# Performance work log

Measured on AMD Instinct MI355X. Metric: run time of the kernel, lower is better.

Reference implementation:

```python
import jax, jax.numpy as jnp
import numpy as np

EMBED = 768
HEADS = 12
HEAD_DIM = EMBED // HEADS
HIDDEN = int(EMBED * 4.0)
EPS = 1e-5


def setup_inputs() -> dict:
    key = jax.random.key(0)
    ks = jax.random.split(key, 12)
    s = 0.02
    return {
        "x": jax.random.normal(ks[0], (8, 1024, EMBED), dtype=jnp.float32),
        # norm1 / norm2 (LayerNorm affine params)
        "g1": jnp.ones((EMBED,), jnp.float32),
        "b1": jnp.zeros((EMBED,), jnp.float32),
        "g2": jnp.ones((EMBED,), jnp.float32),
        "b2": jnp.zeros((EMBED,), jnp.float32),
        # attention weights (stored [in, out]; qkv_bias=False)
        "w_qkv": jax.random.normal(ks[1], (EMBED, 3 * EMBED), jnp.float32) * s,
        "w_proj": jax.random.normal(ks[2], (EMBED, EMBED), jnp.float32) * s,
        "b_proj": jnp.zeros((EMBED,), jnp.float32),
        # MLP weights
        "w_fc1": jax.random.normal(ks[3], (EMBED, HIDDEN), jnp.float32) * s,
        "b_fc1": jnp.zeros((HIDDEN,), jnp.float32),
        "w_fc2": jax.random.normal(ks[4], (HIDDEN, EMBED), jnp.float32) * s,
        "b_fc2": jnp.zeros((EMBED,), jnp.float32),
    }


def _layernorm(x, g, b):
    mu = jnp.mean(x, axis=-1, keepdims=True)
    var = jnp.var(x, axis=-1, keepdims=True)
    return (x - mu) * jax.lax.rsqrt(var + EPS) * g + b


def reference(x, g1, b1, g2, b2, w_qkv, w_proj, b_proj, w_fc1, b_fc1, w_fc2, b_fc2):
    B, N, C = x.shape
    scaling = HEAD_DIM ** (-0.5)

    # --- attention branch ---
    h = _layernorm(x, g1, b1)
    qkv = (h @ w_qkv).reshape(B, N, 3, HEADS, HEAD_DIM)
    q, k, v = qkv[:, :, 0], qkv[:, :, 1], qkv[:, :, 2]  # [B, N, H, D]
    attn = jnp.einsum("bnhd,bmhd->bhnm", q, k) * scaling  # full NxN scores
    attn = jax.nn.softmax(attn, axis=-1)
    out = jnp.einsum("bhnm,bmhd->bnhd", attn, v).reshape(B, N, C)
    out = out @ w_proj + b_proj
    x = x + out

    # --- MLP branch ---
    h = _layernorm(x, g2, b2)
    h = jax.nn.gelu(h @ w_fc1 + b_fc1, approximate=False)
    h = h @ w_fc2 + b_fc2
    return x + h
```

## Files before the change

### kernel.cpp

```cpp
#include <hip/hip_runtime.h>
#include <hip/hip_bf16.h>
#include <math.h>

#define EMBED 768
#define HEADS 12
#define HEAD_DIM 64
#define HIDDEN 3072
#define SEQ 1024
#define BATCH 8
#define TOKENS (SEQ*BATCH)

typedef unsigned short u16;
typedef __attribute__((ext_vector_type(8))) short bf16x8;
typedef __attribute__((ext_vector_type(4))) float floatx4;
typedef __attribute__((ext_vector_type(4))) u16 u16x4;
typedef __attribute__((ext_vector_type(2))) u16 u16x2;

__device__ __forceinline__ u16 f2bf(float f){
    union { float f; unsigned u; } v; v.f = f;
    unsigned r = v.u + 0x7fffu + ((v.u >> 16) & 1u);
    return (u16)(r >> 16);
}

__device__ __forceinline__ unsigned cvt_pk_bf16(float lo, float hi){
    unsigned r;
    asm("v_cvt_pk_bf16_f32 %0, %1, %2" : "=v"(r) : "v"(lo), "v"(hi));
    return r;
}

__device__ __forceinline__ void gload16(const void* g, void* l){
    __builtin_amdgcn_global_load_lds((const __attribute__((address_space(1))) void*)g,
                                     (__attribute__((address_space(3))) void*)l, 16, 0, 0);
}

__device__ __forceinline__ float gelu_fast(float x){
    float t = 1.5957691216f * (x + 0.044715f * x * x * x);
    return x / (1.0f + __expf(-t));
}

__global__ __launch_bounds__(256) void prep_kernel(const float* __restrict__ w0, const float* __restrict__ w1,
                                   const float* __restrict__ w2, const float* __restrict__ w3,
                                   u16* __restrict__ o0, u16* __restrict__ o1,
                                   u16* __restrict__ o2, u16* __restrict__ o3,
                                   const float* __restrict__ x, const float* __restrict__ g,
                                   const float* __restrict__ bln, u16* __restrict__ lnout){
    int bb = blockIdx.x;
    int tid = threadIdx.x;
    if(bb >= 6912){
        int row  = (bb - 6912) * 4 + (tid >> 6);
        int lane = tid & 63;
        const float4* xr = (const float4*)(x + (size_t)row * EMBED);
        float4 v[3];
        float s = 0.f;
        #pragma unroll
        for(int i=0;i<3;i++){
            v[i] = xr[i*64 + lane];
            s += v[i].x + v[i].y + v[i].z + v[i].w;
        }
        #pragma unroll
        for(int o=32;o>0;o>>=1) s += __shfl_xor(s, o);
        float mu = s * (1.0f/EMBED);
        float s2 = 0.f;
        #pragma unroll
        for(int i=0;i<3;i++){
            float dx = v[i].x-mu, dy = v[i].y-mu, dz = v[i].z-mu, dw = v[i].w-mu;
            s2 += dx*dx + dy*dy + dz*dz + dw*dw;
        }
        #pragma unroll
        for(int o=32;o>0;o>>=1) s2 += __shfl_xor(s2, o);
        float rstd = rsqrtf(s2*(1.0f/EMBED) + 1e-5f);
        u16* orow = lnout + (size_t)row * EMBED;
        const float4* g4 = (const float4*)g;
        const float4* b4 = (const float4*)bln;
        #pragma unroll
        for(int i=0;i<3;i++){
            int c4 = i*64 + lane;
            float4 gv = g4[c4], bv = b4[c4];
            u16x4 pk;
            pk.x = f2bf((v[i].x-mu)*rstd*gv.x + bv.x);
            pk.y = f2bf((v[i].y-mu)*rstd*gv.y + bv.y);
            pk.z = f2bf((v[i].z-mu)*rstd*gv.z + bv.z);
            pk.w = f2bf((v[i].w-mu)*rstd*gv.w + bv.w);
            *(u16x4*)(orow + c4*4) = pk;
        }
        return;
    }
    const float* W; u16* Wt; int K, N, bx, by;
    if(bb < 1728)      { int l = bb;        W=w0; Wt=o0; K=768;  N=2304; bx=l%72; by=l/72; }
    else if(bb < 2304) { int l = bb-1728;   W=w1; Wt=o1; K=768;  N=768;  bx=l%24; by=l/24; }
    else if(bb < 4608) { int l = bb-2304;   W=w2; Wt=o2; K=768;  N=3072; bx=l%96; by=l/96; }
    else               { int l = bb-4608;   W=w3; Wt=o3; K=3072; N=768;  bx=l%24; by=l/24; }

    __shared__ float tile[32][33];
    int n0 = bx * 32, k0 = by * 32;
    int tx = tid & 31, ty = tid >> 5;
    #pragma unroll
    for(int i=0;i<32;i+=8) tile[ty+i][tx] = W[(size_t)(k0+ty+i)*N + n0+tx];
    __syncthreads();
    int kp = (tid & 15)*2, nn = tid >> 4;
    #pragma unroll
    for(int p=0;p<2;p++){
        int n = nn + p*16;
        u16x2 w2v;
        w2v.x = f2bf(tile[kp  ][n]);
        w2v.y = f2bf(tile[kp+1][n]);
        *(u16x2*)(Wt + (size_t)(n0+n)*K + k0 + kp) = w2v;
    }
}

__global__ __launch_bounds__(256) void ln_kernel(const float* __restrict__ x, const float* __restrict__ g,
                                                 const float* __restrict__ b, u16* __restrict__ out){
    int row  = blockIdx.x * 4 + (threadIdx.x >> 6);
    int lane = threadIdx.x & 63;
    const float4* xr = (const float4*)(x + (size_t)row * EMBED);
    float4 v[3];
    float s = 0.f;
    #pragma unroll
    for(int i=0;i<3;i++){
        v[i] = xr[i*64 + lane];
        s += v[i].x + v[i].y + v[i].z + v[i].w;
    }
    #pragma unroll
    for(int o=32;o>0;o>>=1) s += __shfl_xor(s, o);
    float mu = s * (1.0f/EMBED);
    float s2 = 0.f;
    #pragma unroll
    for(int i=0;i<3;i++){
        float dx = v[i].x-mu, dy = v[i].y-mu, dz = v[i].z-mu, dw = v[i].w-mu;
        s2 += dx*dx + dy*dy + dz*dz + dw*dw;
    }
    #pragma unroll
    for(int o=32;o>0;o>>=1) s2 += __shfl_xor(s2, o);
    float rstd = rsqrtf(s2*(1.0f/EMBED) + 1e-5f);
    u16* orow = out + (size_t)row * EMBED;
    const float4* g4 = (const float4*)g;
    const float4* b4 = (const float4*)b;
    #pragma unroll
    for(int i=0;i<3;i++){
        int c4 = i*64 + lane;
        float4 gv = g4[c4], bv = b4[c4];
        u16x4 pk;
        pk.x = f2bf((v[i].x-mu)*rstd*gv.x + bv.x);
        pk.y = f2bf((v[i].y-mu)*rstd*gv.y + bv.y);
        pk.z = f2bf((v[i].z-mu)*rstd*gv.z + bv.z);
        pk.w = f2bf((v[i].w-mu)*rstd*gv.w + bv.w);
        *(u16x4*)(orow + c4*4) = pk;
    }
}

template<int EPI>
__global__ __launch_bounds__(512,4) void gemm_wide(const u16* __restrict__ A, const u16* __restrict__ Bt,
        void* __restrict__ Cout, const float* __restrict__ bias, const float* __restrict__ res,
        u16* __restrict__ vt, int M, int N, int K, int ldc){
    __shared__ __align__(16) u16 As[128*64];
    __shared__ __align__(16) u16 Bs[2*256*64];
    int tid  = threadIdx.x;
    int wave = tid >> 6, lane = tid & 63;
    int quad = lane >> 4, lm = lane & 15;
    int wm = (wave >> 2) * 64;
    int wn = (wave & 3) * 64;

    int gx = gridDim.x;
    int bid = blockIdx.y * gx + blockIdx.x;
    int nwg = gx * gridDim.y;
    int cpx = nwg >> 3;
    int swz = (bid & 7) * cpx + (bid >> 3);
    int m0 = (swz / gx) * 128, n0 = (swz % gx) * 256;

    floatx4 acc[4][4];
    #pragma unroll
    for(int i=0;i<4;i++)
        #pragma unroll
        for(int j=0;j<4;j++) acc[i][j] = (floatx4){0.f,0.f,0.f,0.f};

    int srow = tid >> 3;
    int scol = ((tid & 7) ^ (srow & 7)) * 8;
    const u16* aP[2];
    const u16* bP[4];
    #pragma unroll
    for(int p=0;p<2;p++) aP[p] = A  + (size_t)(m0 + p*64 + srow) * K + scol;
    #pragma unroll
    for(int p=0;p<4;p++) bP[p] = Bt + (size_t)(n0 + p*64 + srow) * K + scol;

    int nt = K / 64;
    #pragma unroll
    for(int p=0;p<4;p++) gload16(bP[p], Bs + p*4096 + tid*8);

    for(int t=0; t<nt; ++t){
        int cur = t & 1, nxt = cur ^ 1;
        size_t k0 = (size_t)t * 64;
        #pragma unroll
        for(int p=0;p<2;p++) gload16(aP[p] + k0, As + p*4096 + tid*8);
        if(t+1 < nt){
            #pragma unroll
            for(int p=0;p<4;p++) gload16(bP[p] + k0 + 64, Bs + nxt*16384 + p*4096 + tid*8);
            asm volatile("s_waitcnt vmcnt(4)" ::: "memory");
        } else {
            asm volatile("s_waitcnt vmcnt(0)" ::: "memory");
        }
        __builtin_amdgcn_s_barrier();
        const u16* Bc = Bs + cur*16384;
        #pragma unroll
        for(int ks=0;ks<2;ks++){
            int slotoff = (((ks*4+quad) ^ (lm&7)) << 3);
            bf16x8 af[4], bfr[4];
            #pragma unroll
            for(int i=0;i<4;i++)
                af[i]  = *(const bf16x8*)(As + (wm + i*16 + lm)*64 + slotoff);
            #pragma unroll
            for(int i=0;i<4;i++)
                bfr[i] = *(const bf16x8*)(Bc + (wn + i*16 + lm)*64 + slotoff);
            #pragma unroll
            for(int mf=0;mf<4;mf++)
                #pragma unroll
                for(int nf=0;nf<4;nf++)
                    acc[mf][nf] = __builtin_amdgcn_mfma_f32_16x16x32_bf16(af[mf], bfr[nf], acc[mf][nf], 0, 0, 0);
        }
        __builtin_amdgcn_s_barrier();
    }

    if(EPI == 3 && n0 >= 1536){
        #pragma unroll
        for(int nf=0;nf<4;nf++){
            int col = n0 + wn + nf*16 + lm;
            int hh = (col - 1536) >> 6;
            int d  = col & 63;
            #pragma unroll
            for(int mf=0;mf<4;mf++){
                int row0 = m0 + wm + mf*16 + quad*4;
                int bb  = row0 >> 10;
                int key = row0 & 1023;
                u16x4 pk;
                #pragma unroll
                for(int r=0;r<4;r++) pk[r] = f2bf(acc[mf][nf][r]);
                *(u16x4*)(vt + ((size_t)(bb*HEADS+hh)*64 + d)*SEQ + key) = pk;
            }
        }
        return;
    }

    float bvv[4];
    #pragma unroll
    for(int nf=0;nf<4;nf++) bvv[nf] = bias ? bias[n0 + wn + nf*16 + lm] : 0.f;
    #pragma unroll
    for(int mf=0;mf<4;mf++){
        int row0 = m0 + wm + mf*16 + quad*4;
        #pragma unroll
        for(int r=0;r<4;r++){
            size_t rowoff = (size_t)(row0 + r) * ldc;
            #pragma unroll
            for(int nf=0;nf<4;nf++){
                int col = n0 + wn + nf*16 + lm;
                float v = acc[mf][nf][r] + bvv[nf];
                if(EPI == 1) v = gelu_fast(v);
                if(EPI == 3 && col < 768) v *= 0.18033688011112186f;
                ((u16*)Cout)[rowoff + col] = f2bf(v);
            }
        }
    }
}

template<int EPI>
__global__ __launch_bounds__(256,4) void gemm_nar(const u16* __restrict__ A, const u16* __restrict__ Bt,
        void* __restrict__ Cout, const float* __restrict__ bias, const float* __restrict__ res,
        u16* __restrict__ vt, int M, int N, int K, int ldc){
    constexpr int ASZ = 64*64;
    constexpr int BSZ = 128*64;
    __shared__ __align__(16) u16 As[2*ASZ];
    __shared__ __align__(16) u16 Bs[2*BSZ];
    int tid  = threadIdx.x;
    int wave = tid >> 6, lane = tid & 63;
    int quad = lane >> 4, lm = lane & 15;

    int gx = gridDim.x;
    int bid = blockIdx.y * gx + blockIdx.x;
    int nwg = gx * gridDim.y;
    int cpx = nwg >> 3;
    int swz = (bid & 7) * cpx + (bid >> 3);
    int m0 = (swz / gx) * 64, n0 = (swz % gx) * 128;

    int wm = (wave & 1) * 32;
    int wn = (wave >> 1) * 64;

    floatx4 acc[2][4];
    #pragma unroll
    for(int i=0;i<2;i++)
        #pragma unroll
        for(int j=0;j<4;j++) acc[i][j] = (floatx4){0.f,0.f,0.f,0.f};

    int srow = tid >> 3;
    int scol = ((tid & 7) ^ (srow & 7)) * 8;
    const u16* aP[2];
    const u16* bP[4];
    #pragma unroll
    for(int p=0;p<2;p++) aP[p] = A  + (size_t)(m0 + p*32 + srow) * K + scol;
    #pragma unroll
    for(int p=0;p<4;p++)  bP[p] = Bt + (size_t)(n0 + p*32 + srow) * K + scol;

    int nt = K / 64;
    #pragma unroll
    for(int p=0;p<2;p++) gload16(aP[p], As + p*2048 + tid*8);
    #pragma unroll
    for(int p=0;p<4;p++) gload16(bP[p], Bs + p*2048 + tid*8);

    for(int t=0; t<nt; ++t){
        int cur = t & 1, nxt = cur ^ 1;
        if(t+1 < nt){
            size_t ko = (size_t)(t+1) * 64;
            #pragma unroll
            for(int p=0;p<2;p++) gload16(aP[p] + ko, As + nxt*ASZ + p*2048 + tid*8);
            #pragma unroll
            for(int p=0;p<4;p++) gload16(bP[p] + ko, Bs + nxt*BSZ + p*2048 + tid*8);
            asm volatile("s_waitcnt vmcnt(6)" ::: "memory");
        } else {
            asm volatile("s_waitcnt vmcnt(0)" ::: "memory");
        }
        __builtin_amdgcn_s_barrier();
        const u16* Ac = As + cur*ASZ;
        const u16* Bc = Bs + cur*BSZ;
        #pragma unroll
        for(int ks=0;ks<2;ks++){
            int slotoff = (((ks*4+quad) ^ (lm&7)) << 3);
            bf16x8 af[2], bfr[4];
            #pragma unroll
            for(int i=0;i<2;i++)
                af[i]  = *(const bf16x8*)(Ac + (wm + i*16 + lm)*64 + slotoff);
            #pragma unroll
            for(int i=0;i<4;i++)
                bfr[i] = *(const bf16x8*)(Bc + (wn + i*16 + lm)*64 + slotoff);
            #pragma unroll
            for(int mf=0;mf<2;mf++)
                #pragma unroll
                for(int nf=0;nf<4;nf++)
                    acc[mf][nf] = __builtin_amdgcn_mfma_f32_16x16x32_bf16(af[mf], bfr[nf], acc[mf][nf], 0, 0, 0);
        }
        __builtin_amdgcn_s_barrier();
    }

    float bvv[4];
    #pragma unroll
    for(int nf=0;nf<4;nf++) bvv[nf] = bias ? bias[n0 + wn + nf*16 + lm] : 0.f;
    #pragma unroll
    for(int mf=0;mf<2;mf++){
        int row0 = m0 + wm + mf*16 + quad*4;
        #pragma unroll
        for(int r=0;r<4;r++){
            size_t rowoff = (size_t)(row0 + r) * ldc;
            #pragma unroll
            for(int nf=0;nf<4;nf++){
                int col = n0 + wn + nf*16 + lm;
                float v = acc[mf][nf][r] + bvv[nf];
                if(EPI == 2){
                    ((float*)Cout)[rowoff + col] = v + res[rowoff + col];
                } else {
                    ((u16*)Cout)[rowoff + col] = f2bf(v);
                }
            }
        }
    }
}

__global__ __launch_bounds__(256) void attn_kernel(const u16* __restrict__ qk, const u16* __restrict__ vt,
                                                   u16* __restrict__ out){
    int bid = blockIdx.x;
    int hb = bid % 96;
    int qt = bid / 96;
    int h = hb % HEADS, b = hb / HEADS;
    int tid = threadIdx.x;
    int wave = tid >> 6, lane = tid & 63;
    int quad = lane >> 4, lm = lane & 15;

    __shared__ __align__(16) u16 Ks[2*64*64];
    __shared__ __align__(16) u16 Vs[2*64*64];
    __shared__ __align__(16) u16 P[4*32*64];

    const u16* qbase = qk + (size_t)b * SEQ * 1536;
    const u16* vbase = vt + (size_t)(b*HEADS + h) * 64 * SEQ;
    u16* Pw = P + wave*2048;

    int q0 = qt*128 + wave*32;
    bf16x8 qf[2][2];
    #pragma unroll
    for(int qi=0;qi<2;qi++){
        const u16* qp = qbase + (size_t)(q0 + qi*16 + lm)*1536 + h*64;
        qf[qi][0] = *(const bf16x8*)(qp + quad*8);
        qf[qi][1] = *(const bf16x8*)(qp + 32 + quad*8);
    }

    float l_i[2] = {0.f, 0.f};
    floatx4 o_acc[2][4];
    #pragma unroll
    for(int qi=0;qi<2;qi++)
        #pragma unroll
        for(int nf=0;nf<4;nf++) o_acc[qi][nf] = (floatx4){0.f,0.f,0.f,0.f};

    int sr = lane >> 3;
    int sp = lane & 7;

    auto stage = [&](int kt, int buf){
        #pragma unroll
        for(int i=0;i<2;i++){
            int rr = wave*16 + i*8 + sr;
            int sw = (sp ^ (rr & 7)) * 8;
            gload16(qbase + (size_t)(kt*64 + rr)*1536 + 768 + h*64 + sw,
                    Ks + buf*4096 + (wave*16 + i*8)*64 + lane*8);
            gload16(vbase + (size_t)rr*SEQ + kt*64 + sw,
                    Vs + buf*4096 + (wave*16 + i*8)*64 + lane*8);
        }
    };

    stage(0, 0);
    __syncthreads();

    int cur = 0;
    for(int kt=0; kt<16; kt++){
        if(kt < 15) stage(kt+1, cur^1);
        const u16* Ksb = Ks + cur*4096;
        const u16* Vsb = Vs + cur*4096;

        floatx4 s[4][2];
        #pragma unroll
        for(int kf=0;kf<4;kf++){
            int krow = kf*16 + lm;
            bf16x8 k0 = *(const bf16x8*)(Ksb + krow*64 + ((quad     ^ (lm&7))*8));
            bf16x8 k1 = *(const bf16x8*)(Ksb + krow*64 + (((4+quad) ^ (lm&7))*8));
            #pragma unroll
            for(int qi=0;qi<2;qi++){
                floatx4 t = (floatx4){0.f,0.f,0.f,0.f};
                t = __builtin_amdgcn_mfma_f32_16x16x32_bf16(k0, qf[qi][0], t, 0, 0, 0);
                t = __builtin_amdgcn_mfma_f32_16x16x32_bf16(k1, qf[qi][1], t, 0, 0, 0);
                s[kf][qi] = t;
            }
        }

        #pragma unroll
        for(int qi=0;qi<2;qi++){
            float part = 0.f;
            #pragma unroll
            for(int kf=0;kf<4;kf++){
                #pragma unroll
                for(int r=0;r<4;r++){
                    float e = exp2f(s[kf][qi][r]);
                    s[kf][qi][r] = e;
                    part += e;
                }
            }
            l_i[qi] += part;
            #pragma unroll
            for(int kf=0;kf<4;kf++){
                uint2 pk2;
                pk2.x = cvt_pk_bf16(s[kf][qi][0], s[kf][qi][1]);
                pk2.y = cvt_pk_bf16(s[kf][qi][2], s[kf][qi][3]);
                int c  = kf*4 + quad;
                int cp = c ^ (2*(lm & 7));
                *(uint2*)(Pw + (qi*16 + lm)*64 + cp*4) = pk2;
            }
        }

        #pragma unroll
        for(int ks=0;ks<2;ks++){
            bf16x8 vf[4];
            #pragma unroll
            for(int nf=0;nf<4;nf++)
                vf[nf] = *(const bf16x8*)(Vsb + (nf*16+lm)*64 + (((ks*4+quad) ^ (lm&7))*8));
            #pragma unroll
            for(int qi=0;qi<2;qi++){
                int cr = (ks*8 + 2*quad) ^ (2*(lm & 7));
                bf16x8 pa = *(const bf16x8*)(Pw + (qi*16 + lm)*64 + cr*4);
                #pragma unroll
                for(int nf=0;nf<4;nf++)
                    o_acc[qi][nf] = __builtin_amdgcn_mfma_f32_16x16x32_bf16(pa, vf[nf], o_acc[qi][nf], 0, 0, 0);
            }
        }
        if(kt < 15) __syncthreads();
        cur ^= 1;
    }

    #pragma unroll
    for(int qi=0;qi<2;qi++){
        float lf = l_i[qi];
        lf += __shfl_xor(lf, 16);
        lf += __shfl_xor(lf, 32);
        float rl[4];
        #pragma unroll
        for(int r=0;r<4;r++) rl[r] = 1.0f / __shfl(lf, quad*4 + r);
        int token = b*SEQ + qt*128 + wave*32 + qi*16 + quad*4;
        #pragma unroll
        for(int r=0;r<4;r++){
            size_t rowoff = (size_t)(token + r)*EMBED + h*64;
            #pragma unroll
            for(int nf=0;nf<4;nf++){
                out[rowoff + nf*16 + lm] = f2bf(o_acc[qi][nf][r] * rl[r]);
            }
        }
    }
}

extern "C" void kernel_launch(void* const* d_in, const int* in_sizes, int n_in,
                              void* d_out, int out_size, void* d_ws, size_t ws_size,
                              hipStream_t stream) {
    const float* x      = (const float*)d_in[0];
    const float* g1     = (const float*)d_in[1];
    const float* b1     = (const float*)d_in[2];
    const float* g2     = (const float*)d_in[3];
    const float* b2     = (const float*)d_in[4];
    const float* w_qkv  = (const float*)d_in[5];
    const float* w_proj = (const float*)d_in[6];
    const float* b_proj = (const float*)d_in[7];
    const float* w_fc1  = (const float*)d_in[8];
    const float* b_fc1  = (const float*)d_in[9];
    const float* w_fc2  = (const float*)d_in[10];
    const float* b_fc2  = (const float*)d_in[11];
    float* out = (float*)d_out;

    char* ws = (char*)d_ws;
    u16*   wqkv_t  = (u16*)  (ws + 0);
    u16*   wproj_t = (u16*)  (ws + 3538944);
    u16*   wfc1_t  = (u16*)  (ws + 4718592);
    u16*   wfc2_t  = (u16*)  (ws + 9437184);
    float* x1      = (float*)(ws + 14155776);
    u16*   hbuf    = (u16*)  (ws + 39321600);
    u16*   qkbuf   = (u16*)  (ws + 51904512);
    u16*   vtbuf   = (u16*)  (ws + 77070336);
    u16*   attn_o  = (u16*)  (ws + 89653248);
    u16*   fc1_o   = qkbuf;
    u16*   h2      = hbuf;

    prep_kernel<<<8960, 256, 0, stream>>>(w_qkv, w_proj, w_fc1, w_fc2,
                                          wqkv_t, wproj_t, wfc1_t, wfc2_t,
                                          x, g1, b1, hbuf);

    gemm_wide<3><<<dim3(2304/256, TOKENS/128), 512, 0, stream>>>(hbuf, wqkv_t, qkbuf, nullptr, nullptr, vtbuf, TOKENS, 2304, 768, 1536);

    attn_kernel<<<768, 256, 0, stream>>>(qkbuf, vtbuf, attn_o);

    gemm_nar<2><<<dim3( 768/128, TOKENS/64), 256, 0, stream>>>(attn_o, wproj_t, x1, b_proj, x, nullptr, TOKENS, 768, 768, 768);

    ln_kernel<<<TOKENS/4, 256, 0, stream>>>(x1, g2, b2, h2);

    gemm_wide<1><<<dim3(3072/256, TOKENS/128), 512, 0, stream>>>(h2, wfc1_t, fc1_o, b_fc1, nullptr, nullptr, TOKENS, 3072, 768, 3072);

    gemm_nar<2><<<dim3( 768/128, TOKENS/64), 256, 0, stream>>>(fc1_o, wfc2_t, out, b_fc2, x1, nullptr, TOKENS, 768, 3072, 768);
}
```

Before: 335.1 us.

## Stage attention K/V tiles through registers with single LDS buffer and setprio

Replaces the double-buffered direct global-to-LDS K/V staging in the attention kernel with a register-prefetch scheme. The next tile is loaded into registers during compute, then written to a single LDS buffer between two barriers. This halves the K/V shared memory, which could raise occupancy. It also wraps the MFMA sections in s_setprio to favour matrix issue. The cost is an extra barrier per iteration and more register pressure.

```diff
diff --git a/kernel.cpp b/kernel.cpp
--- a/kernel.cpp
+++ b/kernel.cpp
@@ -370,8 +370,8 @@
     int wave = tid >> 6, lane = tid & 63;
     int quad = lane >> 4, lm = lane & 15;
 
-    __shared__ __align__(16) u16 Ks[2*64*64];
-    __shared__ __align__(16) u16 Vs[2*64*64];
+    __shared__ __align__(16) u16 Ks[64*64];
+    __shared__ __align__(16) u16 Vs[64*64];
     __shared__ __align__(16) u16 P[4*32*64];
 
     const u16* qbase = qk + (size_t)b * SEQ * 1536;
@@ -397,33 +397,47 @@
     int sr = lane >> 3;
     int sp = lane & 7;
 
-    auto stage = [&](int kt, int buf){
-        #pragma unroll
-        for(int i=0;i<2;i++){
-            int rr = wave*16 + i*8 + sr;
-            int sw = (sp ^ (rr & 7)) * 8;
-            gload16(qbase + (size_t)(kt*64 + rr)*1536 + 768 + h*64 + sw,
-                    Ks + buf*4096 + (wave*16 + i*8)*64 + lane*8);
-            gload16(vbase + (size_t)rr*SEQ + kt*64 + sw,
-                    Vs + buf*4096 + (wave*16 + i*8)*64 + lane*8);
-        }
-    };
-
-    stage(0, 0);
+    const u16* ksrc0[2]; const u16* vsrc0[2];
+    u16* kdst[2]; u16* vdst[2];
+    #pragma unroll
+    for(int i=0;i<2;i++){
+        int rr = wave*16 + i*8 + sr;
+        int sw = (sp ^ (rr & 7)) * 8;
+        ksrc0[i] = qbase + (size_t)rr*1536 + 768 + h*64 + sw;
+        vsrc0[i] = vbase + (size_t)rr*SEQ + sw;
+        kdst[i]  = Ks + (wave*16 + i*8)*64 + lane*8;
+        vdst[i]  = Vs + (wave*16 + i*8)*64 + lane*8;
+    }
+
+    uint4 krg[2], vrg[2];
+    #pragma unroll
+    for(int i=0;i<2;i++){
+        krg[i] = *(const uint4*)(ksrc0[i]);
+        vrg[i] = *(const uint4*)(vsrc0[i]);
+    }
+    #pragma unroll
+    for(int i=0;i<2;i++){
+        *(uint4*)kdst[i] = krg[i];
+        *(uint4*)vdst[i] = vrg[i];
+    }
     __syncthreads();
 
-    int cur = 0;
     for(int kt=0; kt<16; kt++){
-        if(kt < 15) stage(kt+1, cur^1);
-        const u16* Ksb = Ks + cur*4096;
-        const u16* Vsb = Vs + cur*4096;
+        if(kt < 15){
+            #pragma unroll
+            for(int i=0;i<2;i++){
+                krg[i] = *(const uint4*)(ksrc0[i] + (size_t)(kt+1)*64*1536);
+                vrg[i] = *(const uint4*)(vsrc0[i] + (kt+1)*64);
+            }
+        }
 
         floatx4 s[4][2];
+        __builtin_amdgcn_s_setprio(1);
         #pragma unroll
         for(int kf=0;kf<4;kf++){
             int krow = kf*16 + lm;
-            bf16x8 k0 = *(const bf16x8*)(Ksb + krow*64 + ((quad     ^ (lm&7))*8));
-            bf16x8 k1 = *(const bf16x8*)(Ksb + krow*64 + (((4+quad) ^ (lm&7))*8));
+            bf16x8 k0 = *(const bf16x8*)(Ks + krow*64 + ((quad     ^ (lm&7))*8));
+            bf16x8 k1 = *(const bf16x8*)(Ks + krow*64 + (((4+quad) ^ (lm&7))*8));
             #pragma unroll
             for(int qi=0;qi<2;qi++){
                 floatx4 t = (floatx4){0.f,0.f,0.f,0.f};
@@ -432,6 +446,7 @@
                 s[kf][qi] = t;
             }
         }
+        __builtin_amdgcn_s_setprio(0);
 
         #pragma unroll
         for(int qi=0;qi<2;qi++){
@@ -457,12 +472,13 @@
             }
         }
 
+        __builtin_amdgcn_s_setprio(1);
         #pragma unroll
         for(int ks=0;ks<2;ks++){
             bf16x8 vf[4];
             #pragma unroll
             for(int nf=0;nf<4;nf++)
-                vf[nf] = *(const bf16x8*)(Vsb + (nf*16+lm)*64 + (((ks*4+quad) ^ (lm&7))*8));
+                vf[nf] = *(const bf16x8*)(Vs + (nf*16+lm)*64 + (((ks*4+quad) ^ (lm&7))*8));
             #pragma unroll
             for(int qi=0;qi<2;qi++){
                 int cr = (ks*8 + 2*quad) ^ (2*(lm & 7));
@@ -472,8 +488,17 @@
                     o_acc[qi][nf] = __builtin_amdgcn_mfma_f32_16x16x32_bf16(pa, vf[nf], o_acc[qi][nf], 0, 0, 0);
             }
         }
-        if(kt < 15) __syncthreads();
-        cur ^= 1;
+        __builtin_amdgcn_s_setprio(0);
+
+        if(kt < 15){
+            __syncthreads();
+            #pragma unroll
+            for(int i=0;i<2;i++){
+                *(uint4*)kdst[i] = krg[i];
+                *(uint4*)vdst[i] = vrg[i];
+            }
+            __syncthreads();
+        }
     }
 
     #pragma unroll
```

Result: slower. 361.7 us (+8.0%).
